# Kernel tuning notes

Hardware: AMD Instinct MI355X
Metric: run time of the kernel (lower is better)

The kernel has to match this reference:

```python
import jax, jax.numpy as jnp
import numpy as np

B, S, D_IN, D_H, D_OUT = 8, 4096, 512, 1024, 512


def setup_inputs() -> dict:
    key = jax.random.key(0)
    ks = jax.random.split(key, 7)
    # scale weights by 1/sqrt(fan_in) so activations stay O(1) through the ReLU stack
    return {
        "query": jax.random.normal(ks[0], (B, S, D_IN), dtype=jnp.float32),
        "W0": jax.random.normal(ks[1], (B, D_H, D_IN), dtype=jnp.float32) * (D_IN ** -0.5),
        "b0": jax.random.normal(ks[2], (B, D_H), dtype=jnp.float32) * 0.02,
        "W1": jax.random.normal(ks[3], (B, D_H, D_H), dtype=jnp.float32) * (D_H ** -0.5),
        "b1": jax.random.normal(ks[4], (B, D_H), dtype=jnp.float32) * 0.02,
        "W2": jax.random.normal(ks[5], (B, D_OUT, D_H), dtype=jnp.float32) * (D_H ** -0.5),
        "b2": jax.random.normal(ks[6], (B, D_OUT), dtype=jnp.float32) * 0.02,
    }


def reference(query, W0, b0, W1, b1, W2, b2):
    # Original loops over (seq, batch) issuing F.linear per sample with per-batch
    # weights; this is exactly a batched GEMM over the batch axis.
    # F.linear(x, w, b) = x @ w.T + b, with w[b] of shape [out, in].
    h = jax.nn.relu(jnp.einsum('bsd,bhd->bsh', query, W0) + b0[:, None, :])  # [B,S,H]
    h = jax.nn.relu(jnp.einsum('bsh,bgh->bsg', h, W1) + b1[:, None, :])      # [B,S,H]
    out = jnp.einsum('bsg,bog->bso', h, W2) + b2[:, None, :]                 # [B,S,O]
    return out
```

## Files before the change

### kernel.cpp

```cpp
#include <hip/hip_runtime.h>


typedef _Float16 f16x8 __attribute__((ext_vector_type(8)));
typedef _Float16 f16x4 __attribute__((ext_vector_type(4)));
typedef float    f32x4 __attribute__((ext_vector_type(4)));

__device__ __forceinline__ void stage16(const void* g, void* l) {
    __builtin_amdgcn_global_load_lds(
        (const __attribute__((address_space(1))) unsigned int*)g,
        (__attribute__((address_space(3))) unsigned int*)l,
        16, 0, 0);
}

template <int CNT> __device__ __forceinline__ void vmwait() {
    if constexpr (CNT == 8)      asm volatile("s_waitcnt vmcnt(8)" ::: "memory");
    else if constexpr (CNT == 4) asm volatile("s_waitcnt vmcnt(4)" ::: "memory");
    else                         asm volatile("s_waitcnt vmcnt(0)" ::: "memory");
}
__device__ __forceinline__ void barrier_() {
    asm volatile("s_barrier" ::: "memory");
}

__device__ __forceinline__ void cast_seg(const float* __restrict__ s,
                                         _Float16* __restrict__ d, int n4) {
    const int stride = gridDim.x * 256;
    for (int i = blockIdx.x * 256 + threadIdx.x; i < n4; i += stride) {
        float4 f = reinterpret_cast<const float4*>(s)[i];
        f16x4 o;
        o[0] = (_Float16)f.x; o[1] = (_Float16)f.y;
        o[2] = (_Float16)f.z; o[3] = (_Float16)f.w;
        reinterpret_cast<f16x4*>(d)[i] = o;
    }
}

__global__ __launch_bounds__(256) void cast_all(
    const float* s0, _Float16* d0, int n0,
    const float* s1, _Float16* d1, int n1,
    const float* s2, _Float16* d2, int n2,
    const float* s3, _Float16* d3, int n3) {
    cast_seg(s0, d0, n0);
    cast_seg(s1, d1, n1);
    cast_seg(s2, d2, n2);
    cast_seg(s3, d3, n3);
}

template <bool RELU, bool OUT_F16>
__global__ __launch_bounds__(512, 2) void gemm_pipe4(
    const _Float16* __restrict__ A, const _Float16* __restrict__ W,
    const float* __restrict__ bias, void* __restrict__ Outv,
    int M, int N, int K) {
    constexpr int BM = 256, BN = 256, BK = 32;
    constexpr int DEPTH = 4;
    __shared__ __align__(16) _Float16 As[DEPTH][BM * BK];
    __shared__ __align__(16) _Float16 Bs[DEPTH][BN * BK];

    const int tid  = threadIdx.x;
    const int lane = tid & 63;
    const int rowl = lane & 15;
    const int qswz = (((lane >> 4) ^ ((rowl >> 1) & 3)) * 8);
    const int w    = tid >> 6;
    const int wm   = (w >> 2) * 128;
    const int wn   = (w & 3) * 64;

    const int bm = blockIdx.x, bn = blockIdx.y, b = blockIdx.z;

    const int c0 = tid, c1 = tid + 512;
    const int ar0 = c0 >> 2, ar1 = c1 >> 2;
    const int ak0 = (((c0 & 3) ^ ((ar0 >> 1) & 3)) * 8);
    const int ak1 = (((c1 & 3) ^ ((ar1 >> 1) & 3)) * 8);

    const char* Ab = (const char*)(A + (size_t)b * M * K + (size_t)(bm * BM) * K);
    const char* Wb = (const char*)(W + (size_t)b * N * K + (size_t)(bn * BN) * K);
    size_t aoff0 = ((size_t)ar0 * K + ak0) * 2;
    size_t aoff1 = ((size_t)ar1 * K + ak1) * 2;
    size_t woff0 = ((size_t)ar0 * K + ak0) * 2;
    size_t woff1 = ((size_t)ar1 * K + ak1) * 2;
    constexpr size_t KSTEP = (size_t)BK * 2;

    f32x4 acc[8][4];
#pragma unroll
    for (int mi = 0; mi < 8; ++mi)
#pragma unroll
        for (int ni = 0; ni < 4; ++ni)
            acc[mi][ni] = (f32x4){0.f, 0.f, 0.f, 0.f};

    const int nk = K / BK;
    const int niter = nk / 2;

#pragma unroll
    for (int p = 0; p < DEPTH - 1; ++p) {
        stage16(Ab + aoff0, &As[p][8 * (size_t)c0]);
        stage16(Ab + aoff1, &As[p][8 * (size_t)c1]);
        stage16(Wb + woff0, &Bs[p][8 * (size_t)c0]);
        stage16(Wb + woff1, &Bs[p][8 * (size_t)c1]);
        aoff0 += KSTEP; aoff1 += KSTEP; woff0 += KSTEP; woff1 += KSTEP;
    }
    vmwait<8>();
    barrier_();

#define BFLOAD(SS)                                                            \
    bf[0] = *(const f16x8*)(&Bs[SS][(wn +  0 + rowl) * BK + qswz]);           \
    bf[1] = *(const f16x8*)(&Bs[SS][(wn + 16 + rowl) * BK + qswz]);           \
    bf[2] = *(const f16x8*)(&Bs[SS][(wn + 32 + rowl) * BK + qswz]);           \
    bf[3] = *(const f16x8*)(&Bs[SS][(wn + 48 + rowl) * BK + qswz]);

#define LDA4(SS, M0)                                                          \
    af[0] = *(const f16x8*)(&As[SS][(wm + ((M0)+0)*16 + rowl) * BK + qswz]);  \
    af[1] = *(const f16x8*)(&As[SS][(wm + ((M0)+1)*16 + rowl) * BK + qswz]);  \
    af[2] = *(const f16x8*)(&As[SS][(wm + ((M0)+2)*16 + rowl) * BK + qswz]);  \
    af[3] = *(const f16x8*)(&As[SS][(wm + ((M0)+3)*16 + rowl) * BK + qswz]);

#define MFMA16(M0)                                                            \
    __builtin_amdgcn_s_setprio(1);                                            \
    acc[(M0)+0][0] = __builtin_amdgcn_mfma_f32_16x16x32_f16(af[0], bf[0], acc[(M0)+0][0], 0, 0, 0); \
    acc[(M0)+0][1] = __builtin_amdgcn_mfma_f32_16x16x32_f16(af[0], bf[1], acc[(M0)+0][1], 0, 0, 0); \
    acc[(M0)+0][2] = __builtin_amdgcn_mfma_f32_16x16x32_f16(af[0], bf[2], acc[(M0)+0][2], 0, 0, 0); \
    acc[(M0)+0][3] = __builtin_amdgcn_mfma_f32_16x16x32_f16(af[0], bf[3], acc[(M0)+0][3], 0, 0, 0); \
    acc[(M0)+1][0] = __builtin_amdgcn_mfma_f32_16x16x32_f16(af[1], bf[0], acc[(M0)+1][0], 0, 0, 0); \
    acc[(M0)+1][1] = __builtin_amdgcn_mfma_f32_16x16x32_f16(af[1], bf[1], acc[(M0)+1][1], 0, 0, 0); \
    acc[(M0)+1][2] = __builtin_amdgcn_mfma_f32_16x16x32_f16(af[1], bf[2], acc[(M0)+1][2], 0, 0, 0); \
    acc[(M0)+1][3] = __builtin_amdgcn_mfma_f32_16x16x32_f16(af[1], bf[3], acc[(M0)+1][3], 0, 0, 0); \
    acc[(M0)+2][0] = __builtin_amdgcn_mfma_f32_16x16x32_f16(af[2], bf[0], acc[(M0)+2][0], 0, 0, 0); \
    acc[(M0)+2][1] = __builtin_amdgcn_mfma_f32_16x16x32_f16(af[2], bf[1], acc[(M0)+2][1], 0, 0, 0); \
    acc[(M0)+2][2] = __builtin_amdgcn_mfma_f32_16x16x32_f16(af[2], bf[2], acc[(M0)+2][2], 0, 0, 0); \
    acc[(M0)+2][3] = __builtin_amdgcn_mfma_f32_16x16x32_f16(af[2], bf[3], acc[(M0)+2][3], 0, 0, 0); \
    acc[(M0)+3][0] = __builtin_amdgcn_mfma_f32_16x16x32_f16(af[3], bf[0], acc[(M0)+3][0], 0, 0, 0); \
    acc[(M0)+3][1] = __builtin_amdgcn_mfma_f32_16x16x32_f16(af[3], bf[1], acc[(M0)+3][1], 0, 0, 0); \
    acc[(M0)+3][2] = __builtin_amdgcn_mfma_f32_16x16x32_f16(af[3], bf[2], acc[(M0)+3][2], 0, 0, 0); \
    acc[(M0)+3][3] = __builtin_amdgcn_mfma_f32_16x16x32_f16(af[3], bf[3], acc[(M0)+3][3], 0, 0, 0); \
    __builtin_amdgcn_s_setprio(0);

    for (int i = 0; i < niter; ++i) {
        const int t0 = 2 * i;
        const int s0 = t0 & 3, s1 = (t0 + 1) & 3;
        const int sA = (t0 + 3) & 3;
        const int sB = s0;
        const bool stg01 = (t0 + 3 < nk);
        const bool stg23 = (t0 + 4 < nk);

        f16x8 bf[4], af[4];

        {
            BFLOAD(s0);
            LDA4(s0, 0);
            if (stg01) {
                stage16(Ab + aoff0, &As[sA][8 * (size_t)c0]);
                stage16(Ab + aoff1, &As[sA][8 * (size_t)c1]);
            }
            barrier_();
            MFMA16(0);
            barrier_();
        }
        {
            LDA4(s0, 4);
            if (stg01) {
                stage16(Wb + woff0, &Bs[sA][8 * (size_t)c0]);
                stage16(Wb + woff1, &Bs[sA][8 * (size_t)c1]);
            }
            barrier_();
            MFMA16(4);
            if (i + 1 < niter) vmwait<8>(); else vmwait<0>();
            barrier_();
        }
        aoff0 += KSTEP; aoff1 += KSTEP; woff0 += KSTEP; woff1 += KSTEP;

        {
            BFLOAD(s1);
            LDA4(s1, 0);
            if (stg23) {
                stage16(Ab + aoff0, &As[sB][8 * (size_t)c0]);
                stage16(Ab + aoff1, &As[sB][8 * (size_t)c1]);
            }
            barrier_();
            MFMA16(0);
            barrier_();
        }
        {
            LDA4(s1, 4);
            if (stg23) {
                stage16(Wb + woff0, &Bs[sB][8 * (size_t)c0]);
                stage16(Wb + woff1, &Bs[sB][8 * (size_t)c1]);
            }
            barrier_();
            MFMA16(4);
            if (i + 2 < niter)      vmwait<8>();
            else if (i + 1 < niter) vmwait<4>();
            barrier_();
        }
        aoff0 += KSTEP; aoff1 += KSTEP; woff0 += KSTEP; woff1 += KSTEP;
    }
#undef BFLOAD
#undef LDA4
#undef MFMA16

    const int q = lane >> 4;
    float bcol[4];
    {
        const float* bp = bias + (size_t)b * N + bn * BN + wn;
#pragma unroll
        for (int ni = 0; ni < 4; ++ni) bcol[ni] = bp[ni * 16 + rowl];
    }
#pragma unroll
    for (int mi = 0; mi < 8; ++mi) {
        const int row0 = bm * BM + wm + mi * 16 + q * 4;
#pragma unroll
        for (int r = 0; r < 4; ++r) {
            const size_t ro = (size_t)b * M * N + (size_t)(row0 + r) * N + bn * BN + wn;
#pragma unroll
            for (int ni = 0; ni < 4; ++ni) {
                float v = acc[mi][ni][r] + bcol[ni];
                if (RELU) v = fmaxf(v, 0.f);
                if (OUT_F16)
                    ((_Float16*)Outv)[ro + ni * 16 + rowl] = (_Float16)v;
                else
                    ((float*)Outv)[ro + ni * 16 + rowl] = v;
            }
        }
    }
}

__device__ __forceinline__ uint4 load8f32(const char* p) {
    const float4* fp = reinterpret_cast<const float4*>(p);
    float4 f0 = fp[0], f1 = fp[1];
    f16x8 o;
    o[0] = (_Float16)f0.x; o[1] = (_Float16)f0.y;
    o[2] = (_Float16)f0.z; o[3] = (_Float16)f0.w;
    o[4] = (_Float16)f1.x; o[5] = (_Float16)f1.y;
    o[6] = (_Float16)f1.z; o[7] = (_Float16)f1.w;
    return __builtin_bit_cast(uint4, o);
}

template <bool A_F16, bool W_F16, bool RELU, bool OUT_F16>
__global__ __launch_bounds__(256) void gemm_bias_act(
    const void* __restrict__ Av, const void* __restrict__ Wv,
    const float* __restrict__ bias, void* __restrict__ Outv,
    int M, int N, int K) {
    constexpr int BM = 128, BN = 128, BK = 32;
    __shared__ __align__(16) _Float16 As[BM * BK];
    __shared__ __align__(16) _Float16 Bs[BN * BK];

    const int tid  = threadIdx.x;
    const int lane = tid & 63;
    const int rowl = lane & 15;
    const int q8   = (lane >> 4) * 8;
    const int wm   = ((tid >> 6) >> 1) * 64;
    const int wn   = ((tid >> 6) & 1) * 64;
    const int bm = blockIdx.x, bn = blockIdx.y, b = blockIdx.z;

    const int c0 = tid, c1 = tid + 256;
    const int ar0 = c0 >> 2, ak0 = (c0 & 3) * 8;
    const int ar1 = c1 >> 2, ak1 = (c1 & 3) * 8;

    constexpr size_t esA = A_F16 ? 2 : 4;
    constexpr size_t esW = W_F16 ? 2 : 4;
    const char* Abase = (const char*)Av;
    const char* Wbase = (const char*)Wv;

    size_t aoff0 = ((size_t)b * M * K + (size_t)(bm * BM + ar0) * K + ak0) * esA;
    size_t aoff1 = ((size_t)b * M * K + (size_t)(bm * BM + ar1) * K + ak1) * esA;
    size_t woff0 = ((size_t)b * N * K + (size_t)(bn * BN + ar0) * K + ak0) * esW;
    size_t woff1 = ((size_t)b * N * K + (size_t)(bn * BN + ar1) * K + ak1) * esW;

    f32x4 acc[4][4];
#pragma unroll
    for (int mi = 0; mi < 4; ++mi)
#pragma unroll
        for (int ni = 0; ni < 4; ++ni)
            acc[mi][ni] = (f32x4){0.f, 0.f, 0.f, 0.f};

    const int nk = K / BK;
    for (int kk = 0; kk < nk; ++kk) {
        uint4 va0, va1, vw0, vw1;
        if (!A_F16) { va0 = load8f32(Abase + aoff0); va1 = load8f32(Abase + aoff1); }
        if (!W_F16) { vw0 = load8f32(Wbase + woff0); vw1 = load8f32(Wbase + woff1); }
        __syncthreads();
        if (A_F16) {
            stage16(Abase + aoff0, As + 8 * (size_t)c0);
            stage16(Abase + aoff1, As + 8 * (size_t)c1);
        } else {
            *(uint4*)(As + ar0 * BK + ak0) = va0;
            *(uint4*)(As + ar1 * BK + ak1) = va1;
        }
        if (W_F16) {
            stage16(Wbase + woff0, Bs + 8 * (size_t)c0);
            stage16(Wbase + woff1, Bs + 8 * (size_t)c1);
        } else {
            *(uint4*)(Bs + ar0 * BK + ak0) = vw0;
            *(uint4*)(Bs + ar1 * BK + ak1) = vw1;
        }
        aoff0 += BK * esA; aoff1 += BK * esA;
        woff0 += BK * esW; woff1 += BK * esW;
        __syncthreads();

        f16x8 af[4], bf[4];
#pragma unroll
        for (int i = 0; i < 4; ++i)
            af[i] = *(const f16x8*)(As + (wm + i * 16 + rowl) * BK + q8);
#pragma unroll
        for (int i = 0; i < 4; ++i)
            bf[i] = *(const f16x8*)(Bs + (wn + i * 16 + rowl) * BK + q8);
#pragma unroll
        for (int mi = 0; mi < 4; ++mi)
#pragma unroll
            for (int ni = 0; ni < 4; ++ni)
                acc[mi][ni] = __builtin_amdgcn_mfma_f32_16x16x32_f16(
                    af[mi], bf[ni], acc[mi][ni], 0, 0, 0);
    }

    const int q = lane >> 4;
    float bcol[4];
    {
        const float* bp = bias + (size_t)b * N + bn * BN + wn;
#pragma unroll
        for (int ni = 0; ni < 4; ++ni) bcol[ni] = bp[ni * 16 + rowl];
    }
#pragma unroll
    for (int mi = 0; mi < 4; ++mi) {
        const int row0 = bm * BM + wm + mi * 16 + q * 4;
#pragma unroll
        for (int r = 0; r < 4; ++r) {
            const size_t ro = (size_t)b * M * N + (size_t)(row0 + r) * N + bn * BN + wn;
#pragma unroll
            for (int ni = 0; ni < 4; ++ni) {
                float v = acc[mi][ni][r] + bcol[ni];
                if (RELU) v = fmaxf(v, 0.f);
                if (OUT_F16)
                    ((_Float16*)Outv)[ro + ni * 16 + rowl] = (_Float16)v;
                else
                    ((float*)Outv)[ro + ni * 16 + rowl] = v;
            }
        }
    }
}

extern "C" void kernel_launch(void* const* d_in, const int* in_sizes, int n_in,
                              void* d_out, int out_size, void* d_ws, size_t ws_size,
                              hipStream_t stream) {
    const int B = 8, S = 4096, DI = 512, DH = 1024, DO = 512;
    const float* query = (const float*)d_in[0];
    const float* W0    = (const float*)d_in[1];
    const float* b0    = (const float*)d_in[2];
    const float* W1    = (const float*)d_in[3];
    const float* b1    = (const float*)d_in[4];
    const float* W2    = (const float*)d_in[5];
    const float* b2    = (const float*)d_in[6];

    char* ws = (char*)d_ws;
    const size_t nH  = (size_t)B * S * DH;
    const size_t nQ  = (size_t)B * S * DI;
    const size_t nW0 = (size_t)B * DH * DI;
    const size_t nW1 = (size_t)B * DH * DH;
    const size_t nW2 = (size_t)B * DO * DH;

    _Float16* h0 = (_Float16*)ws;
    _Float16* h1 = (_Float16*)(ws + nH * 2);
    const size_t off_casts = nH * 4;
    const size_t full_need = off_casts + (nQ + nW0 + nW1 + nW2) * 2;

    if (ws_size >= full_need) {
        _Float16* qf  = (_Float16*)(ws + off_casts);
        _Float16* w0f = qf + nQ;
        _Float16* w1f = w0f + nW0;
        _Float16* w2f = w1f + nW1;
        cast_all<<<dim3(2048), dim3(256), 0, stream>>>(
            query, qf, (int)(nQ / 4), W0, w0f, (int)(nW0 / 4),
            W1, w1f, (int)(nW1 / 4), W2, w2f, (int)(nW2 / 4));
        const dim3 blk(512);
        const dim3 g0(S / 256, DH / 256, B);
        const dim3 g2(S / 256, DO / 256, B);
        gemm_pipe4<true,  true ><<<g0, blk, 0, stream>>>(qf, w0f, b0, h0, S, DH, DI);
        gemm_pipe4<true,  true ><<<g0, blk, 0, stream>>>(h0, w1f, b1, h1, S, DH, DH);
        gemm_pipe4<false, false><<<g2, blk, 0, stream>>>(h1, w2f, b2, d_out, S, DO, DH);
    } else {
        const dim3 blk(256);
        const dim3 g0(S / 128, DH / 128, B);
        const dim3 g2(S / 128, DO / 128, B);
        gemm_bias_act<false, false, true,  true ><<<g0, blk, 0, stream>>>(query, W0, b0, h0, S, DH, DI);
        gemm_bias_act<true,  false, true,  true ><<<g0, blk, 0, stream>>>(h0, W1, b1, h1, S, DH, DH);
        gemm_bias_act<true,  false, false, false><<<g2, blk, 0, stream>>>(h1, W2, b2, d_out, S, DO, DH);
    }
}
```

Before: 337.0 us.

## Double-buffer LDS fragment registers to overlap ds_reads with MFMA

The GEMM main loop is restructured so the A/B fragments for the next half-tile are read from LDS into a second register set while the current set feeds the MFMAs. This removes the barrier that previously separated each LDS read from its MFMA block, leaving one barrier per quarter step. The global-to-LDS staging is reordered and the vmcnt waits are retuned to match. The cost is more VGPR pressure, which may cause spills under the 512x2 launch bound, and a more fragile stage-reuse ordering.

```diff
diff --git a/kernel.cpp b/kernel.cpp
--- a/kernel.cpp
+++ b/kernel.cpp
@@ -14,6 +14,7 @@
 
 template <int CNT> __device__ __forceinline__ void vmwait() {
     if constexpr (CNT == 8)      asm volatile("s_waitcnt vmcnt(8)" ::: "memory");
+    else if constexpr (CNT == 6) asm volatile("s_waitcnt vmcnt(6)" ::: "memory");
     else if constexpr (CNT == 4) asm volatile("s_waitcnt vmcnt(4)" ::: "memory");
     else                         asm volatile("s_waitcnt vmcnt(0)" ::: "memory");
 }
@@ -45,7 +46,7 @@
 }
 
 template <bool RELU, bool OUT_F16>
-__global__ __launch_bounds__(512, 2) void gemm_pipe4(
+__global__ __launch_bounds__(512, 2) void gemm_rpipe(
     const _Float16* __restrict__ A, const _Float16* __restrict__ W,
     const float* __restrict__ bias, void* __restrict__ Outv,
     int M, int N, int K) {
@@ -98,99 +99,97 @@
     vmwait<8>();
     barrier_();
 
-#define BFLOAD(SS)                                                            \
-    bf[0] = *(const f16x8*)(&Bs[SS][(wn +  0 + rowl) * BK + qswz]);           \
-    bf[1] = *(const f16x8*)(&Bs[SS][(wn + 16 + rowl) * BK + qswz]);           \
-    bf[2] = *(const f16x8*)(&Bs[SS][(wn + 32 + rowl) * BK + qswz]);           \
-    bf[3] = *(const f16x8*)(&Bs[SS][(wn + 48 + rowl) * BK + qswz]);
-
-#define LDA4(SS, M0)                                                          \
-    af[0] = *(const f16x8*)(&As[SS][(wm + ((M0)+0)*16 + rowl) * BK + qswz]);  \
-    af[1] = *(const f16x8*)(&As[SS][(wm + ((M0)+1)*16 + rowl) * BK + qswz]);  \
-    af[2] = *(const f16x8*)(&As[SS][(wm + ((M0)+2)*16 + rowl) * BK + qswz]);  \
-    af[3] = *(const f16x8*)(&As[SS][(wm + ((M0)+3)*16 + rowl) * BK + qswz]);
-
-#define MFMA16(M0)                                                            \
-    __builtin_amdgcn_s_setprio(1);                                            \
-    acc[(M0)+0][0] = __builtin_amdgcn_mfma_f32_16x16x32_f16(af[0], bf[0], acc[(M0)+0][0], 0, 0, 0); \
-    acc[(M0)+0][1] = __builtin_amdgcn_mfma_f32_16x16x32_f16(af[0], bf[1], acc[(M0)+0][1], 0, 0, 0); \
-    acc[(M0)+0][2] = __builtin_amdgcn_mfma_f32_16x16x32_f16(af[0], bf[2], acc[(M0)+0][2], 0, 0, 0); \
-    acc[(M0)+0][3] = __builtin_amdgcn_mfma_f32_16x16x32_f16(af[0], bf[3], acc[(M0)+0][3], 0, 0, 0); \
-    acc[(M0)+1][0] = __builtin_amdgcn_mfma_f32_16x16x32_f16(af[1], bf[0], acc[(M0)+1][0], 0, 0, 0); \
-    acc[(M0)+1][1] = __builtin_amdgcn_mfma_f32_16x16x32_f16(af[1], bf[1], acc[(M0)+1][1], 0, 0, 0); \
-    acc[(M0)+1][2] = __builtin_amdgcn_mfma_f32_16x16x32_f16(af[1], bf[2], acc[(M0)+1][2], 0, 0, 0); \
-    acc[(M0)+1][3] = __builtin_amdgcn_mfma_f32_16x16x32_f16(af[1], bf[3], acc[(M0)+1][3], 0, 0, 0); \
-    acc[(M0)+2][0] = __builtin_amdgcn_mfma_f32_16x16x32_f16(af[2], bf[0], acc[(M0)+2][0], 0, 0, 0); \
-    acc[(M0)+2][1] = __builtin_amdgcn_mfma_f32_16x16x32_f16(af[2], bf[1], acc[(M0)+2][1], 0, 0, 0); \
-    acc[(M0)+2][2] = __builtin_amdgcn_mfma_f32_16x16x32_f16(af[2], bf[2], acc[(M0)+2][2], 0, 0, 0); \
-    acc[(M0)+2][3] = __builtin_amdgcn_mfma_f32_16x16x32_f16(af[2], bf[3], acc[(M0)+2][3], 0, 0, 0); \
-    acc[(M0)+3][0] = __builtin_amdgcn_mfma_f32_16x16x32_f16(af[3], bf[0], acc[(M0)+3][0], 0, 0, 0); \
-    acc[(M0)+3][1] = __builtin_amdgcn_mfma_f32_16x16x32_f16(af[3], bf[1], acc[(M0)+3][1], 0, 0, 0); \
-    acc[(M0)+3][2] = __builtin_amdgcn_mfma_f32_16x16x32_f16(af[3], bf[2], acc[(M0)+3][2], 0, 0, 0); \
-    acc[(M0)+3][3] = __builtin_amdgcn_mfma_f32_16x16x32_f16(af[3], bf[3], acc[(M0)+3][3], 0, 0, 0); \
+    f16x8 afA[4], afB[4], bfA[4], bfB[4];
+
+#define LDAF(DST, SS, M0)                                                        \
+    DST[0] = *(const f16x8*)(&As[SS][(wm + ((M0)+0)*16 + rowl) * BK + qswz]);    \
+    DST[1] = *(const f16x8*)(&As[SS][(wm + ((M0)+1)*16 + rowl) * BK + qswz]);    \
+    DST[2] = *(const f16x8*)(&As[SS][(wm + ((M0)+2)*16 + rowl) * BK + qswz]);    \
+    DST[3] = *(const f16x8*)(&As[SS][(wm + ((M0)+3)*16 + rowl) * BK + qswz]);
+
+#define LDBF(DST, SS)                                                            \
+    DST[0] = *(const f16x8*)(&Bs[SS][(wn +  0 + rowl) * BK + qswz]);             \
+    DST[1] = *(const f16x8*)(&Bs[SS][(wn + 16 + rowl) * BK + qswz]);             \
+    DST[2] = *(const f16x8*)(&Bs[SS][(wn + 32 + rowl) * BK + qswz]);             \
+    DST[3] = *(const f16x8*)(&Bs[SS][(wn + 48 + rowl) * BK + qswz]);
+
+#define MFMA16(AF, BF, M0)                                                       \
+    __builtin_amdgcn_s_setprio(1);                                               \
+    acc[(M0)+0][0] = __builtin_amdgcn_mfma_f32_16x16x32_f16(AF[0], BF[0], acc[(M0)+0][0], 0, 0, 0); \
+    acc[(M0)+0][1] = __builtin_amdgcn_mfma_f32_16x16x32_f16(AF[0], BF[1], acc[(M0)+0][1], 0, 0, 0); \
+    acc[(M0)+0][2] = __builtin_amdgcn_mfma_f32_16x16x32_f16(AF[0], BF[2], acc[(M0)+0][2], 0, 0, 0); \
+    acc[(M0)+0][3] = __builtin_amdgcn_mfma_f32_16x16x32_f16(AF[0], BF[3], acc[(M0)+0][3], 0, 0, 0); \
+    acc[(M0)+1][0] = __builtin_amdgcn_mfma_f32_16x16x32_f16(AF[1], BF[0], acc[(M0)+1][0], 0, 0, 0); \
+    acc[(M0)+1][1] = __builtin_amdgcn_mfma_f32_16x16x32_f16(AF[1], BF[1], acc[(M0)+1][1], 0, 0, 0); \
+    acc[(M0)+1][2] = __builtin_amdgcn_mfma_f32_16x16x32_f16(AF[1], BF[2], acc[(M0)+1][2], 0, 0, 0); \
+    acc[(M0)+1][3] = __builtin_amdgcn_mfma_f32_16x16x32_f16(AF[1], BF[3], acc[(M0)+1][3], 0, 0, 0); \
+    acc[(M0)+2][0] = __builtin_amdgcn_mfma_f32_16x16x32_f16(AF[2], BF[0], acc[(M0)+2][0], 0, 0, 0); \
+    acc[(M0)+2][1] = __builtin_amdgcn_mfma_f32_16x16x32_f16(AF[2], BF[1], acc[(M0)+2][1], 0, 0, 0); \
+    acc[(M0)+2][2] = __builtin_amdgcn_mfma_f32_16x16x32_f16(AF[2], BF[2], acc[(M0)+2][2], 0, 0, 0); \
+    acc[(M0)+2][3] = __builtin_amdgcn_mfma_f32_16x16x32_f16(AF[2], BF[3], acc[(M0)+2][3], 0, 0, 0); \
+    acc[(M0)+3][0] = __builtin_amdgcn_mfma_f32_16x16x32_f16(AF[3], BF[0], acc[(M0)+3][0], 0, 0, 0); \
+    acc[(M0)+3][1] = __builtin_amdgcn_mfma_f32_16x16x32_f16(AF[3], BF[1], acc[(M0)+3][1], 0, 0, 0); \
+    acc[(M0)+3][2] = __builtin_amdgcn_mfma_f32_16x16x32_f16(AF[3], BF[2], acc[(M0)+3][2], 0, 0, 0); \
+    acc[(M0)+3][3] = __builtin_amdgcn_mfma_f32_16x16x32_f16(AF[3], BF[3], acc[(M0)+3][3], 0, 0, 0); \
     __builtin_amdgcn_s_setprio(0);
+
+    LDBF(bfA, 0);
+    LDAF(afA, 0, 0);
 
     for (int i = 0; i < niter; ++i) {
         const int t0 = 2 * i;
-        const int s0 = t0 & 3, s1 = (t0 + 1) & 3;
+        const int s0 = t0 & 3, s1 = (t0 + 1) & 3, s2 = (t0 + 2) & 3;
         const int sA = (t0 + 3) & 3;
         const int sB = s0;
-        const bool stg01 = (t0 + 3 < nk);
-        const bool stg23 = (t0 + 4 < nk);
-
-        f16x8 bf[4], af[4];
-
-        {
-            BFLOAD(s0);
-            LDA4(s0, 0);
-            if (stg01) {
-                stage16(Ab + aoff0, &As[sA][8 * (size_t)c0]);
-                stage16(Ab + aoff1, &As[sA][8 * (size_t)c1]);
-            }
-            barrier_();
-            MFMA16(0);
-            barrier_();
-        }
-        {
-            LDA4(s0, 4);
-            if (stg01) {
-                stage16(Wb + woff0, &Bs[sA][8 * (size_t)c0]);
-                stage16(Wb + woff1, &Bs[sA][8 * (size_t)c1]);
-            }
-            barrier_();
-            MFMA16(4);
-            if (i + 1 < niter) vmwait<8>(); else vmwait<0>();
-            barrier_();
-        }
-        aoff0 += KSTEP; aoff1 += KSTEP; woff0 += KSTEP; woff1 += KSTEP;
-
-        {
-            BFLOAD(s1);
-            LDA4(s1, 0);
-            if (stg23) {
-                stage16(Ab + aoff0, &As[sB][8 * (size_t)c0]);
-                stage16(Ab + aoff1, &As[sB][8 * (size_t)c1]);
-            }
-            barrier_();
-            MFMA16(0);
-            barrier_();
-        }
-        {
-            LDA4(s1, 4);
-            if (stg23) {
-                stage16(Wb + woff0, &Bs[sB][8 * (size_t)c0]);
-                stage16(Wb + woff1, &Bs[sB][8 * (size_t)c1]);
-            }
-            barrier_();
-            MFMA16(4);
-            if (i + 2 < niter)      vmwait<8>();
-            else if (i + 1 < niter) vmwait<4>();
-            barrier_();
-        }
-        aoff0 += KSTEP; aoff1 += KSTEP; woff0 += KSTEP; woff1 += KSTEP;
-    }
-#undef BFLOAD
-#undef LDA4
+        const bool stgO = (t0 + 3 < nk);
+        const bool stgE = (t0 + 4 < nk);
+        const bool last = (i + 1 == niter);
+
+        barrier_();
+        LDAF(afB, s0, 4);
+        if (stgO) {
+            stage16(Ab + aoff0, &As[sA][8 * (size_t)c0]);
+            stage16(Ab + aoff1, &As[sA][8 * (size_t)c1]);
+        }
+        aoff0 += KSTEP; aoff1 += KSTEP;
+        MFMA16(afA, bfA, 0);
+        if (!last) vmwait<6>(); else vmwait<0>();
+
+        barrier_();
+        LDBF(bfB, s1);
+        LDAF(afA, s1, 0);
+        if (stgO) {
+            stage16(Wb + woff0, &Bs[sA][8 * (size_t)c0]);
+            stage16(Wb + woff1, &Bs[sA][8 * (size_t)c1]);
+        }
+        woff0 += KSTEP; woff1 += KSTEP;
+        MFMA16(afB, bfA, 4);
+
+        barrier_();
+        LDAF(afB, s1, 4);
+        if (stgE) {
+            stage16(Wb + woff0, &Bs[sB][8 * (size_t)c0]);
+            stage16(Wb + woff1, &Bs[sB][8 * (size_t)c1]);
+        }
+        woff0 += KSTEP; woff1 += KSTEP;
+        MFMA16(afA, bfB, 0);
+        if (i + 2 < niter)      vmwait<6>();
+        else if (i + 1 < niter) vmwait<4>();
+
+        barrier_();
+        if (!last) {
+            LDBF(bfA, s2);
+            LDAF(afA, s2, 0);
+        }
+        if (stgE) {
+            stage16(Ab + aoff0, &As[sB][8 * (size_t)c0]);
+            stage16(Ab + aoff1, &As[sB][8 * (size_t)c1]);
+        }
+        aoff0 += KSTEP; aoff1 += KSTEP;
+        MFMA16(afB, bfB, 4);
+    }
+#undef LDAF
+#undef LDBF
 #undef MFMA16
 
     const int q = lane >> 4;
@@ -368,9 +367,9 @@
         const dim3 blk(512);
         const dim3 g0(S / 256, DH / 256, B);
         const dim3 g2(S / 256, DO / 256, B);
-        gemm_pipe4<true,  true ><<<g0, blk, 0, stream>>>(qf, w0f, b0, h0, S, DH, DI);
-        gemm_pipe4<true,  true ><<<g0, blk, 0, stream>>>(h0, w1f, b1, h1, S, DH, DH);
-        gemm_pipe4<false, false><<<g2, blk, 0, stream>>>(h1, w2f, b2, d_out, S, DO, DH);
+        gemm_rpipe<true,  true ><<<g0, blk, 0, stream>>>(qf, w0f, b0, h0, S, DH, DI);
+        gemm_rpipe<true,  true ><<<g0, blk, 0, stream>>>(h0, w1f, b1, h1, S, DH, DH);
+        gemm_rpipe<false, false><<<g2, blk, 0, stream>>>(h1, w2f, b2, d_out, S, DO, DH);
     } else {
         const dim3 blk(256);
         const dim3 g0(S / 128, DH / 128, B);
```

Result: faster. 328.6 us (-2.5%).
